# Kernel optimization log

Measured on AMD Instinct MI355X. Metric: run time of the kernel, lower is better.

## Reference

```python
import jax, jax.numpy as jnp
import numpy as np

HIDDEN = 1024
NUM_HEADS = 16
HEAD_DIM = HIDDEN // NUM_HEADS


def setup_inputs() -> dict:
    key = jax.random.key(0)
    k1, k2, k3 = jax.random.split(key, 3)
    x = jax.random.normal(k1, (2, 2048, HIDDEN), dtype=jnp.float32)
    # Linear weights, torch layout [out_features, in_features]
    w_qkv = jax.random.normal(k2, (3 * HIDDEN, HIDDEN), dtype=jnp.float32) * 0.02
    w_out = jax.random.normal(k3, (HIDDEN, HIDDEN), dtype=jnp.float32) * 0.02
    return {"x": x, "w_qkv": w_qkv, "w_out": w_out}


def reference(x, w_qkv, w_out):
    B, S, H = x.shape
    scale = 1.0 / HEAD_DIM ** 0.5
    qkv = jnp.einsum('bsh,oh->bso', x, w_qkv)              # [B,S,3H]
    qkv = qkv.reshape(B, S, 3, NUM_HEADS, HEAD_DIM)
    qkv = jnp.transpose(qkv, (2, 0, 3, 1, 4))               # [3,B,nh,S,hd]
    q, k, v = qkv[0], qkv[1], qkv[2]
    scores = jnp.einsum('bnsd,bntd->bnst', q, k) * scale    # [B,nh,S,S]
    attn = jax.nn.softmax(scores, axis=-1)
    out = jnp.einsum('bnst,bntd->bnsd', attn, v)            # [B,nh,S,hd]
    out = jnp.transpose(out, (0, 2, 1, 3)).reshape(B, S, H)
    return jnp.einsum('bsh,oh->bso', out, w_out)
```

## Files before the change

### kernel.cpp

```cpp
#include <hip/hip_runtime.h>
#include <stdint.h>

typedef unsigned short u16;
typedef __bf16 bf16x8 __attribute__((ext_vector_type(8)));
typedef float f32x4 __attribute__((ext_vector_type(4)));
typedef float f32x16 __attribute__((ext_vector_type(16)));
typedef unsigned u32x4 __attribute__((ext_vector_type(4)));

#define DEVI __device__ __forceinline__

typedef __attribute__((address_space(1))) void gvoid;
typedef __attribute__((address_space(3))) void lvoid;

DEVI u16 f2b(float f) {
  unsigned x = __builtin_bit_cast(unsigned, f);
  return (u16)((x + 0x7fffu + ((x >> 16) & 1u)) >> 16);
}

DEVI float exp2g(float x) { return __builtin_amdgcn_exp2f(x); }

DEVI void gload_lds16(const void* g, void* l) {
  __builtin_amdgcn_global_load_lds((gvoid*)g, (lvoid*)l, 16, 0, 0);
}

#define QSCALE 0.18033688011112042f

__global__ void cast_all(const float* __restrict__ x, const float* __restrict__ wqkv,
                         const float* __restrict__ wout, u16* __restrict__ outb) {
  int i = blockIdx.x * 256 + threadIdx.x;
  int stride = gridDim.x * 256;
  for (; i < 2097152; i += stride) {
    const float* src;
    float sc = 1.0f;
    if (i < 1048576) {
      src = x + 4 * (long)i;
    } else if (i < 1835008) {
      int j = i - 1048576;
      src = wqkv + 4 * (long)j;
      if (j < 262144) sc = QSCALE;
    } else {
      src = wout + 4 * (long)(i - 1835008);
    }
    float4 v = *(const float4*)src;
    ushort4 o;
    o.x = f2b(v.x * sc); o.y = f2b(v.y * sc); o.z = f2b(v.z * sc); o.w = f2b(v.w * sc);
    ((ushort4*)outb)[i] = o;
  }
}

template<int OUT, int TM>
__global__ __launch_bounds__(256)
void gemm_bt(const u16* __restrict__ A, const u16* __restrict__ B, void* __restrict__ Cv,
             void* __restrict__ Cv2, int M, int N, int K) {
  constexpr int MI = TM / 32;
  __shared__ u16 lA[TM * 64];
  __shared__ u16 lB[128 * 64];
  const int tid = threadIdx.x;
  const int lane = tid & 63;
  const int lr = lane & 15;
  const int lg = lane >> 4;
  const int wid = tid >> 6;
  const long bm = (long)blockIdx.y * TM;
  const long bn = (long)blockIdx.x * 128;
  const int wr = (wid >> 1) * (TM / 2);
  const int wc = (wid & 1) * 64;

  f32x4 acc[MI][4];
#pragma unroll
  for (int i = 0; i < MI; ++i)
#pragma unroll
    for (int j = 0; j < 4; ++j)
      acc[i][j] = (f32x4){0.f, 0.f, 0.f, 0.f};

  for (int k0 = 0; k0 < K; k0 += 64) {
#pragma unroll
    for (int q = 0; q < MI; ++q) {
      int bi = tid + q * 256;
      int row = bi >> 3;
      int col = ((bi & 7) ^ (row & 7)) * 8;
      gload_lds16(A + (bm + row) * (long)K + k0 + col, (char*)lA + bi * 16);
    }
#pragma unroll
    for (int q = 0; q < 4; ++q) {
      int bi = tid + q * 256;
      int row = bi >> 3;
      int col = ((bi & 7) ^ (row & 7)) * 8;
      gload_lds16(B + (bn + row) * (long)K + k0 + col, (char*)lB + bi * 16);
    }
    __syncthreads();
#pragma unroll
    for (int kk = 0; kk < 2; ++kk) {
      bf16x8 af[MI], bfr[4];
      int kb = kk * 4 + lg;
#pragma unroll
      for (int mi = 0; mi < MI; ++mi) {
        int row = wr + mi * 16 + lr;
        af[mi] = *(const bf16x8*)((const char*)lA + row * 128 + ((kb ^ (row & 7)) << 4));
      }
#pragma unroll
      for (int ni = 0; ni < 4; ++ni) {
        int row = wc + ni * 16 + lr;
        bfr[ni] = *(const bf16x8*)((const char*)lB + row * 128 + ((kb ^ (row & 7)) << 4));
      }
#pragma unroll
      for (int mi = 0; mi < MI; ++mi)
#pragma unroll
        for (int ni = 0; ni < 4; ++ni)
          acc[mi][ni] = __builtin_amdgcn_mfma_f32_16x16x32_bf16(af[mi], bfr[ni], acc[mi][ni], 0, 0, 0);
    }
    __syncthreads();
  }

  if (OUT == 2 && bn >= 2048) {
#pragma unroll
    for (int mi = 0; mi < MI; ++mi)
#pragma unroll
      for (int ni = 0; ni < 4; ++ni) {
        long tok = bm + wr + mi * 16 + lg * 4;
        long f = bn + wc + ni * 16 + lr - 2048;
        ushort4 st;
        st.x = f2b(acc[mi][ni][0]);
        st.y = f2b(acc[mi][ni][1]);
        st.z = f2b(acc[mi][ni][2]);
        st.w = f2b(acc[mi][ni][3]);
        u16* dst = (u16*)Cv2 + (((tok >> 11) << 4) + (f >> 6)) * 131072 + (f & 63) * 2048 + (tok & 2047);
        *(ushort4*)dst = st;
      }
  } else {
    const long strideN = (OUT == 2) ? 2048 : N;
#pragma unroll
    for (int mi = 0; mi < MI; ++mi)
#pragma unroll
      for (int ni = 0; ni < 4; ++ni)
#pragma unroll
        for (int r = 0; r < 4; ++r) {
          long row = bm + wr + mi * 16 + lg * 4 + r;
          long col = bn + wc + ni * 16 + lr;
          float v = acc[mi][ni][r];
          if (OUT == 1) ((float*)Cv)[row * strideN + col] = v;
          else          ((u16*)Cv)[row * strideN + col] = f2b(v);
        }
  }
}

__global__ __launch_bounds__(256, 4)
void attn_fwd(const u16* __restrict__ qk, const u16* __restrict__ vT,
              u16* __restrict__ outb) {
  __shared__ char SM[32768];

  const int tid = threadIdx.x;
  const int lane = tid & 63;
  const int wid = tid >> 6;
  const int ql = lane & 31;
  const int h  = lane >> 5;
  const int th = wid >> 1;
  const int qb = wid & 1;

  const int flat = blockIdx.x + (blockIdx.y << 5) + (blockIdx.z << 9);
  const int swz  = ((flat & 7) << 7) + (flat >> 3);
  const int qt = swz & 31;
  const int hd = (swz >> 5) & 15;
  const int b  = swz >> 9;

  const long rowbase = (long)b * 2048;
  const int qcol = hd * 64;
  const int kcol = 1024 + hd * 64;
  const int TSK = 64 * 2048;
  const long vhb = ((long)b * 16 + hd) * 131072;

  const int q0w = qt * 64 + qb * 32;
  bf16x8 qf[4];
  {
    const u16* qp = qk + (rowbase + q0w + ql) * 2048 + qcol + h * 8;
#pragma unroll
    for (int dblk = 0; dblk < 4; ++dblk)
      qf[dblk] = *(const bf16x8*)(qp + dblk * 16);
  }

  float l_r = 0.f;
  f32x16 o[2];
#pragma unroll
  for (int d = 0; d < 2; ++d)
#pragma unroll
    for (int r = 0; r < 16; ++r) o[d][r] = 0.f;

  const int c0 = tid, c1 = tid + 256;
  const int rk0 = c0 >> 3, ck0 = ((c0 & 7) ^ (rk0 & 7)) * 8;
  const int rk1 = c1 >> 3, ck1 = ((c1 & 7) ^ (rk1 & 7)) * 8;
  const int d0 = c0 * 16, d1 = c1 * 16;
  const u16* kp0 = qk + (rowbase + rk0) * 2048 + kcol + ck0;
  const u16* kp1 = qk + (rowbase + rk1) * 2048 + kcol + ck1;
  const u16* vp0 = vT + vhb + rk0 * 2048 + ck0;
  const u16* vp1 = vT + vhb + rk1 * 2048 + ck1;

  gload_lds16(kp0, SM + d0);          gload_lds16(kp1, SM + d1);
  gload_lds16(vp0, SM + 16384 + d0);  gload_lds16(vp1, SM + 16384 + d1);
  kp0 += TSK; kp1 += TSK; vp0 += 64; vp1 += 64;
  asm volatile("s_waitcnt vmcnt(0)" ::: "memory");
  __builtin_amdgcn_s_barrier();
  __builtin_amdgcn_sched_barrier(0);

  for (int tt = 0; tt < 16; ++tt) {
#pragma unroll
    for (int P = 0; P < 2; ++P) {
      char* KsCur = SM + P * 8192;
      char* VsCur = SM + 16384 + P * 8192;
      char* KsNxt = SM + (P ^ 1) * 8192;
      char* VsNxt = SM + 16384 + (P ^ 1) * 8192;

      gload_lds16(kp0, KsNxt + d0);  gload_lds16(kp1, KsNxt + d1);
      gload_lds16(vp0, VsNxt + d0);  gload_lds16(vp1, VsNxt + d1);
      kp0 += TSK; kp1 += TSK; vp0 += 64; vp1 += 64;

      f32x16 s;
#pragma unroll
      for (int r = 0; r < 16; ++r) s[r] = 0.f;
      const char* Kb = KsCur + (th * 32 + ql) * 128;
      __builtin_amdgcn_s_setprio(1);
#pragma unroll
      for (int kd = 0; kd < 4; ++kd) {
        bf16x8 kf = *(const bf16x8*)(Kb + (((kd * 2 + h) ^ (ql & 7)) << 4));
        s = __builtin_amdgcn_mfma_f32_32x32x16_bf16(kf, qf[kd], s, 0, 0, 0);
      }
      __builtin_amdgcn_s_setprio(0);

#pragma unroll
      for (int r = 0; r < 16; ++r) s[r] = exp2g(s[r]);
      l_r += (((s[0] + s[1]) + (s[2] + s[3])) + ((s[4] + s[5]) + (s[6] + s[7])))
           + (((s[8] + s[9]) + (s[10] + s[11])) + ((s[12] + s[13]) + (s[14] + s[15])));

      unsigned w[8];
#pragma unroll
      for (int m = 0; m < 8; ++m)
        asm("v_cvt_pk_bf16_f32 %0, %1, %2" : "=v"(w[m]) : "v"(s[2 * m]), "v"(s[2 * m + 1]));

      bf16x8 pb[2];
#pragma unroll
      for (int ks = 0; ks < 2; ++ks) {
        unsigned a0 = w[4 * ks],     a2 = w[4 * ks + 2];
        unsigned a1 = w[4 * ks + 1], a3 = w[4 * ks + 3];
        asm("s_nop 1\n\tv_permlane32_swap_b32 %0, %1" : "+v"(a0), "+v"(a2));
        asm("s_nop 1\n\tv_permlane32_swap_b32 %0, %1" : "+v"(a1), "+v"(a3));
        u32x4 t; t[0] = a0; t[1] = a1; t[2] = a2; t[3] = a3;
        pb[ks] = __builtin_bit_cast(bf16x8, t);
      }

      __builtin_amdgcn_s_setprio(1);
#pragma unroll
      for (int dblk = 0; dblk < 2; ++dblk) {
        const char* Vb = VsCur + (dblk * 32 + ql) * 128;
#pragma unroll
        for (int ks = 0; ks < 2; ++ks) {
          bf16x8 vf = *(const bf16x8*)(Vb + (((th * 4 + ks * 2 + h) ^ (ql & 7)) << 4));
          o[dblk] = __builtin_amdgcn_mfma_f32_32x32x16_bf16(vf, pb[ks], o[dblk], 0, 0, 0);
        }
      }
      __builtin_amdgcn_s_setprio(0);

      asm volatile("s_waitcnt vmcnt(0)" ::: "memory");
      __builtin_amdgcn_s_barrier();
      __builtin_amdgcn_sched_barrier(0);
    }
  }
  __syncthreads();

  float px = l_r, py = l_r;
  asm("s_nop 1\n\tv_permlane32_swap_b32 %0, %1" : "+v"(px), "+v"(py));
  float lw = l_r + (h ? px : py);

  if (th == 1) {
    char* reg = SM + qb * 8320;
#pragma unroll
    for (int dblk = 0; dblk < 2; ++dblk)
#pragma unroll
      for (int r = 0; r < 16; ++r) {
        int dl = dblk * 32 + (r & 3) + 8 * (r >> 2) + 4 * h;
        *(float*)(reg + dl * 128 + ql * 4) = o[dblk][r];
      }
    if (h == 0) *(float*)(reg + 8192 + ql * 4) = lw;
  }
  __syncthreads();
  if (th == 0) {
    const char* reg = SM + qb * 8320;
#pragma unroll
    for (int dblk = 0; dblk < 2; ++dblk)
#pragma unroll
      for (int r = 0; r < 16; ++r) {
        int dl = dblk * 32 + (r & 3) + 8 * (r >> 2) + 4 * h;
        o[dblk][r] += *(const float*)(reg + dl * 128 + ql * 4);
      }
    float inv = 1.0f / (lw + *(const float*)(reg + 8192 + ql * 4));
    long row = rowbase + q0w + ql;
#pragma unroll
    for (int dblk = 0; dblk < 2; ++dblk)
#pragma unroll
      for (int m = 0; m < 4; ++m) {
        ushort4 st;
        st.x = f2b(o[dblk][4 * m + 0] * inv);
        st.y = f2b(o[dblk][4 * m + 1] * inv);
        st.z = f2b(o[dblk][4 * m + 2] * inv);
        st.w = f2b(o[dblk][4 * m + 3] * inv);
        *(ushort4*)(outb + row * 1024 + qcol + dblk * 32 + 8 * m + 4 * h) = st;
      }
  }
}

extern "C" void kernel_launch(void* const* d_in, const int* in_sizes, int n_in,
                              void* d_out, int out_size, void* d_ws, size_t ws_size,
                              hipStream_t stream) {
  const float* x     = (const float*)d_in[0];
  const float* w_qkv = (const float*)d_in[1];
  const float* w_out = (const float*)d_in[2];
  float* out = (float*)d_out;

  char* ws = (char*)d_ws;
  u16* xb    = (u16*)(ws);
  u16* wqkvb = (u16*)(ws + 8388608);
  u16* woutb = (u16*)(ws + 14680064);
  u16* qk    = (u16*)(ws + 16777216);
  u16* vT    = (u16*)(ws + 33554432);
  u16* attn  = (u16*)(ws + 41943040);

  cast_all<<<2048, 256, 0, stream>>>(x, w_qkv, w_out, xb);

  gemm_bt<2, 128><<<dim3(24, 32), 256, 0, stream>>>(xb, wqkvb, qk, vT, 4096, 3072, 1024);

  attn_fwd<<<dim3(32, 16, 2), 256, 0, stream>>>(qk, vT, attn);

  gemm_bt<1, 64><<<dim3(8, 64), 256, 0, stream>>>(attn, woutb, out, nullptr, 4096, 1024, 1024);
}
```

Baseline: 106.6 us.

## Process 128 query rows per attention block to reuse K/V tiles twice

Each wave now holds two 32-row query fragments, so every K and V fragment read from LDS feeds two MFMAs. The block covers 128 queries instead of 64 and the grid is halved, which halves the global K/V traffic per query. The cost is roughly double the accumulator and score registers, so launch bounds drop to 2 blocks per CU. Fewer blocks and lower occupancy could hurt latency hiding, and with 512 blocks there may be too few to fill the GPU.

```diff
diff --git a/kernel.cpp b/kernel.cpp
--- a/kernel.cpp
+++ b/kernel.cpp
@@ -143,10 +143,10 @@
   }
 }
 
-__global__ __launch_bounds__(256, 4)
+__global__ __launch_bounds__(256, 2)
 void attn_fwd(const u16* __restrict__ qk, const u16* __restrict__ vT,
               u16* __restrict__ outb) {
-  __shared__ char SM[32768];
+  __shared__ char SM[33280];
 
   const int tid = threadIdx.x;
   const int lane = tid & 63;
@@ -154,13 +154,13 @@
   const int ql = lane & 31;
   const int h  = lane >> 5;
   const int th = wid >> 1;
-  const int qb = wid & 1;
-
-  const int flat = blockIdx.x + (blockIdx.y << 5) + (blockIdx.z << 9);
-  const int swz  = ((flat & 7) << 7) + (flat >> 3);
-  const int qt = swz & 31;
-  const int hd = (swz >> 5) & 15;
-  const int b  = swz >> 9;
+  const int qw = wid & 1;
+
+  const int flat = blockIdx.x + (blockIdx.y << 4) + (blockIdx.z << 8);
+  const int swz  = ((flat & 7) << 6) + (flat >> 3);
+  const int qt = swz & 15;
+  const int hd = (swz >> 4) & 15;
+  const int b  = swz >> 8;
 
   const long rowbase = (long)b * 2048;
   const int qcol = hd * 64;
@@ -168,21 +168,24 @@
   const int TSK = 64 * 2048;
   const long vhb = ((long)b * 16 + hd) * 131072;
 
-  const int q0w = qt * 64 + qb * 32;
-  bf16x8 qf[4];
+  const int q0w = qt * 128 + qw * 64;
+  bf16x8 qfA[4], qfB[4];
   {
-    const u16* qp = qk + (rowbase + q0w + ql) * 2048 + qcol + h * 8;
-#pragma unroll
-    for (int dblk = 0; dblk < 4; ++dblk)
-      qf[dblk] = *(const bf16x8*)(qp + dblk * 16);
-  }
-
-  float l_r = 0.f;
-  f32x16 o[2];
+    const u16* qpA = qk + (rowbase + q0w + ql) * 2048 + qcol + h * 8;
+    const u16* qpB = qpA + 32 * 2048;
+#pragma unroll
+    for (int dblk = 0; dblk < 4; ++dblk) {
+      qfA[dblk] = *(const bf16x8*)(qpA + dblk * 16);
+      qfB[dblk] = *(const bf16x8*)(qpB + dblk * 16);
+    }
+  }
+
+  float lA = 0.f, lB = 0.f;
+  f32x16 oA[2], oB[2];
 #pragma unroll
   for (int d = 0; d < 2; ++d)
 #pragma unroll
-    for (int r = 0; r < 16; ++r) o[d][r] = 0.f;
+    for (int r = 0; r < 16; ++r) { oA[d][r] = 0.f; oB[d][r] = 0.f; }
 
   const int c0 = tid, c1 = tid + 256;
   const int rk0 = c0 >> 3, ck0 = ((c0 & 7) ^ (rk0 & 7)) * 8;
@@ -212,37 +215,50 @@
       gload_lds16(vp0, VsNxt + d0);  gload_lds16(vp1, VsNxt + d1);
       kp0 += TSK; kp1 += TSK; vp0 += 64; vp1 += 64;
 
-      f32x16 s;
-#pragma unroll
-      for (int r = 0; r < 16; ++r) s[r] = 0.f;
+      f32x16 sA, sB;
+#pragma unroll
+      for (int r = 0; r < 16; ++r) { sA[r] = 0.f; sB[r] = 0.f; }
       const char* Kb = KsCur + (th * 32 + ql) * 128;
       __builtin_amdgcn_s_setprio(1);
 #pragma unroll
       for (int kd = 0; kd < 4; ++kd) {
         bf16x8 kf = *(const bf16x8*)(Kb + (((kd * 2 + h) ^ (ql & 7)) << 4));
-        s = __builtin_amdgcn_mfma_f32_32x32x16_bf16(kf, qf[kd], s, 0, 0, 0);
+        sA = __builtin_amdgcn_mfma_f32_32x32x16_bf16(kf, qfA[kd], sA, 0, 0, 0);
+        sB = __builtin_amdgcn_mfma_f32_32x32x16_bf16(kf, qfB[kd], sB, 0, 0, 0);
       }
       __builtin_amdgcn_s_setprio(0);
 
 #pragma unroll
-      for (int r = 0; r < 16; ++r) s[r] = exp2g(s[r]);
-      l_r += (((s[0] + s[1]) + (s[2] + s[3])) + ((s[4] + s[5]) + (s[6] + s[7])))
-           + (((s[8] + s[9]) + (s[10] + s[11])) + ((s[12] + s[13]) + (s[14] + s[15])));
-
-      unsigned w[8];
-#pragma unroll
-      for (int m = 0; m < 8; ++m)
-        asm("v_cvt_pk_bf16_f32 %0, %1, %2" : "=v"(w[m]) : "v"(s[2 * m]), "v"(s[2 * m + 1]));
-
-      bf16x8 pb[2];
+      for (int r = 0; r < 16; ++r) sA[r] = exp2g(sA[r]);
+#pragma unroll
+      for (int r = 0; r < 16; ++r) sB[r] = exp2g(sB[r]);
+      lA += (((sA[0] + sA[1]) + (sA[2] + sA[3])) + ((sA[4] + sA[5]) + (sA[6] + sA[7])))
+          + (((sA[8] + sA[9]) + (sA[10] + sA[11])) + ((sA[12] + sA[13]) + (sA[14] + sA[15])));
+      lB += (((sB[0] + sB[1]) + (sB[2] + sB[3])) + ((sB[4] + sB[5]) + (sB[6] + sB[7])))
+          + (((sB[8] + sB[9]) + (sB[10] + sB[11])) + ((sB[12] + sB[13]) + (sB[14] + sB[15])));
+
+      unsigned wA[8], wB[8];
+#pragma unroll
+      for (int m = 0; m < 8; ++m) {
+        asm("v_cvt_pk_bf16_f32 %0, %1, %2" : "=v"(wA[m]) : "v"(sA[2 * m]), "v"(sA[2 * m + 1]));
+        asm("v_cvt_pk_bf16_f32 %0, %1, %2" : "=v"(wB[m]) : "v"(sB[2 * m]), "v"(sB[2 * m + 1]));
+      }
+
+      bf16x8 pbA[2], pbB[2];
 #pragma unroll
       for (int ks = 0; ks < 2; ++ks) {
-        unsigned a0 = w[4 * ks],     a2 = w[4 * ks + 2];
-        unsigned a1 = w[4 * ks + 1], a3 = w[4 * ks + 3];
+        unsigned a0 = wA[4 * ks],     a2 = wA[4 * ks + 2];
+        unsigned a1 = wA[4 * ks + 1], a3 = wA[4 * ks + 3];
         asm("s_nop 1\n\tv_permlane32_swap_b32 %0, %1" : "+v"(a0), "+v"(a2));
         asm("s_nop 1\n\tv_permlane32_swap_b32 %0, %1" : "+v"(a1), "+v"(a3));
         u32x4 t; t[0] = a0; t[1] = a1; t[2] = a2; t[3] = a3;
-        pb[ks] = __builtin_bit_cast(bf16x8, t);
+        pbA[ks] = __builtin_bit_cast(bf16x8, t);
+        unsigned b0 = wB[4 * ks],     b2 = wB[4 * ks + 2];
+        unsigned b1 = wB[4 * ks + 1], b3 = wB[4 * ks + 3];
+        asm("s_nop 1\n\tv_permlane32_swap_b32 %0, %1" : "+v"(b0), "+v"(b2));
+        asm("s_nop 1\n\tv_permlane32_swap_b32 %0, %1" : "+v"(b1), "+v"(b3));
+        u32x4 u; u[0] = b0; u[1] = b1; u[2] = b2; u[3] = b3;
+        pbB[ks] = __builtin_bit_cast(bf16x8, u);
       }
 
       __builtin_amdgcn_s_setprio(1);
@@ -252,7 +268,8 @@
 #pragma unroll
         for (int ks = 0; ks < 2; ++ks) {
           bf16x8 vf = *(const bf16x8*)(Vb + (((th * 4 + ks * 2 + h) ^ (ql & 7)) << 4));
-          o[dblk] = __builtin_amdgcn_mfma_f32_32x32x16_bf16(vf, pb[ks], o[dblk], 0, 0, 0);
+          oA[dblk] = __builtin_amdgcn_mfma_f32_32x32x16_bf16(vf, pbA[ks], oA[dblk], 0, 0, 0);
+          oB[dblk] = __builtin_amdgcn_mfma_f32_32x32x16_bf16(vf, pbB[ks], oB[dblk], 0, 0, 0);
         }
       }
       __builtin_amdgcn_s_setprio(0);
@@ -264,43 +281,61 @@
   }
   __syncthreads();
 
-  float px = l_r, py = l_r;
-  asm("s_nop 1\n\tv_permlane32_swap_b32 %0, %1" : "+v"(px), "+v"(py));
-  float lw = l_r + (h ? px : py);
+  float pxA = lA, pyA = lA;
+  asm("s_nop 1\n\tv_permlane32_swap_b32 %0, %1" : "+v"(pxA), "+v"(pyA));
+  float lwA = lA + (h ? pxA : pyA);
+  float pxB = lB, pyB = lB;
+  asm("s_nop 1\n\tv_permlane32_swap_b32 %0, %1" : "+v"(pxB), "+v"(pyB));
+  float lwB = lB + (h ? pxB : pyB);
 
   if (th == 1) {
-    char* reg = SM + qb * 8320;
+    char* regA = SM + (qw * 2 + 0) * 8192;
+    char* regB = SM + (qw * 2 + 1) * 8192;
 #pragma unroll
     for (int dblk = 0; dblk < 2; ++dblk)
 #pragma unroll
       for (int r = 0; r < 16; ++r) {
         int dl = dblk * 32 + (r & 3) + 8 * (r >> 2) + 4 * h;
-        *(float*)(reg + dl * 128 + ql * 4) = o[dblk][r];
-      }
-    if (h == 0) *(float*)(reg + 8192 + ql * 4) = lw;
+        *(float*)(regA + dl * 128 + ql * 4) = oA[dblk][r];
+        *(float*)(regB + dl * 128 + ql * 4) = oB[dblk][r];
+      }
+    if (h == 0) {
+      *(float*)(SM + 32768 + (qw * 2 + 0) * 128 + ql * 4) = lwA;
+      *(float*)(SM + 32768 + (qw * 2 + 1) * 128 + ql * 4) = lwB;
+    }
   }
   __syncthreads();
   if (th == 0) {
-    const char* reg = SM + qb * 8320;
+    const char* regA = SM + (qw * 2 + 0) * 8192;
+    const char* regB = SM + (qw * 2 + 1) * 8192;
 #pragma unroll
     for (int dblk = 0; dblk < 2; ++dblk)
 #pragma unroll
       for (int r = 0; r < 16; ++r) {
         int dl = dblk * 32 + (r & 3) + 8 * (r >> 2) + 4 * h;
-        o[dblk][r] += *(const float*)(reg + dl * 128 + ql * 4);
-      }
-    float inv = 1.0f / (lw + *(const float*)(reg + 8192 + ql * 4));
-    long row = rowbase + q0w + ql;
+        oA[dblk][r] += *(const float*)(regA + dl * 128 + ql * 4);
+        oB[dblk][r] += *(const float*)(regB + dl * 128 + ql * 4);
+      }
+    float invA = 1.0f / (lwA + *(const float*)(SM + 32768 + (qw * 2 + 0) * 128 + ql * 4));
+    float invB = 1.0f / (lwB + *(const float*)(SM + 32768 + (qw * 2 + 1) * 128 + ql * 4));
+    long rowA = rowbase + q0w + ql;
+    long rowB = rowA + 32;
 #pragma unroll
     for (int dblk = 0; dblk < 2; ++dblk)
 #pragma unroll
       for (int m = 0; m < 4; ++m) {
-        ushort4 st;
-        st.x = f2b(o[dblk][4 * m + 0] * inv);
-        st.y = f2b(o[dblk][4 * m + 1] * inv);
-        st.z = f2b(o[dblk][4 * m + 2] * inv);
-        st.w = f2b(o[dblk][4 * m + 3] * inv);
-        *(ushort4*)(outb + row * 1024 + qcol + dblk * 32 + 8 * m + 4 * h) = st;
+        ushort4 stA;
+        stA.x = f2b(oA[dblk][4 * m + 0] * invA);
+        stA.y = f2b(oA[dblk][4 * m + 1] * invA);
+        stA.z = f2b(oA[dblk][4 * m + 2] * invA);
+        stA.w = f2b(oA[dblk][4 * m + 3] * invA);
+        *(ushort4*)(outb + rowA * 1024 + qcol + dblk * 32 + 8 * m + 4 * h) = stA;
+        ushort4 stB;
+        stB.x = f2b(oB[dblk][4 * m + 0] * invB);
+        stB.y = f2b(oB[dblk][4 * m + 1] * invB);
+        stB.z = f2b(oB[dblk][4 * m + 2] * invB);
+        stB.w = f2b(oB[dblk][4 * m + 3] * invB);
+        *(ushort4*)(outb + rowB * 1024 + qcol + dblk * 32 + 8 * m + 4 * h) = stB;
       }
   }
 }
@@ -325,7 +360,7 @@
 
   gemm_bt<2, 128><<<dim3(24, 32), 256, 0, stream>>>(xb, wqkvb, qk, vT, 4096, 3072, 1024);
 
-  attn_fwd<<<dim3(32, 16, 2), 256, 0, stream>>>(qk, vT, attn);
+  attn_fwd<<<dim3(16, 16, 2), 256, 0, stream>>>(qk, vT, attn);
 
   gemm_bt<1, 64><<<dim3(8, 64), 256, 0, stream>>>(attn, woutb, out, nullptr, 4096, 1024, 1024);
 }
```

Result: faster. 103.0 us (-3.4%).
